# Performance work log

Hardware: AMD Instinct MI355X
Metric: run time of the kernel (lower is better)

The kernel has to match this reference:

```python
import jax, jax.numpy as jnp
import numpy as np

B, N, C, H = 64, 197, 768, 12
CH = C // H            # 64 head dim
RC = CH // 2           # 32 reduced channel
RN = N // 8            # 24 reduced tokens
TOPK_COEF = 8
BUDGET = int(np.ceil(0.25 * N))   # 50
BASIS_THRESH = 0.02
MP_SCALE = H ** -0.5               # MaskPredictor: num_heads**-0.5 (as in source)
ATTN_SCALE = CH ** -0.5
LN_EPS = 1e-5


def _ln(x, g, b):
    mu = x.mean(-1, keepdims=True)
    var = ((x - mu) ** 2).mean(-1, keepdims=True)
    return (x - mu) * jax.lax.rsqrt(var + LN_EPS) * g + b


def _keep_topk(x, k):
    # zero all but the k largest along last axis (tie-break by value threshold)
    kth = jax.lax.top_k(x, k)[0][..., -1:]
    return jnp.where(x >= kth, x, 0.0)


def setup_inputs() -> dict:
    key = jax.random.key(0)
    ks = jax.random.split(key, 20)
    d = {}
    d['x'] = jax.random.normal(ks[0], (B, N, C), jnp.float32)
    s = 0.02
    d['Wqkv'] = jax.random.normal(ks[1], (C, 3 * C), jnp.float32) * s
    d['Wcq'] = jax.random.normal(ks[2], (CH, RC), jnp.float32) * s
    d['bcq'] = jnp.zeros((RC,), jnp.float32)
    d['Wck'] = jax.random.normal(ks[3], (CH, RC), jnp.float32) * s
    d['bck'] = jnp.zeros((RC,), jnp.float32)
    d['proj_n'] = jax.random.normal(ks[4], (N, RN), jnp.float32) * s
    d['proj_back_n'] = jax.random.normal(ks[5], (N, RN), jnp.float32) * s
    d['Wproj'] = jax.random.normal(ks[6], (C, C), jnp.float32) * s
    d['bproj'] = jnp.zeros((C,), jnp.float32)
    d['g1'] = jnp.ones((C,), jnp.float32)
    d['b1'] = jnp.zeros((C,), jnp.float32)
    d['g2'] = jnp.ones((C,), jnp.float32)
    d['b2'] = jnp.zeros((C,), jnp.float32)
    d['W1'] = jax.random.normal(ks[7], (C, 4 * C), jnp.float32) * s
    d['bfc1'] = jnp.zeros((4 * C,), jnp.float32)
    d['W2'] = jax.random.normal(ks[8], (4 * C, C), jnp.float32) * s
    d['bfc2'] = jnp.zeros((C,), jnp.float32)
    return d


def reference(x, Wqkv, Wcq, bcq, Wck, bck, proj_n, proj_back_n, Wproj, bproj,
              g1, b1, g2, b2, W1, bfc1, W2, bfc2):
    h = _ln(x, g1, b1)
    qkv = (h @ Wqkv).reshape(B, N, 3, H, CH).transpose(2, 0, 3, 1, 4)  # [3,B,H,N,CH]
    q, k, v = qkv[0], qkv[1], qkv[2]

    # ---- MaskPredictor (eval path) ----
    qp = q @ Wcq + bcq                                # [B,H,N,RC]
    kp = k @ Wck + bck                                # [B,H,N,RC]
    kk = jnp.einsum('bhnc,nr->bhcr', kp, proj_n)      # [B,H,RC,RN]
    cheap = jnp.einsum('bhnc,bhcr->bhnr', qp, kk) * MP_SCALE
    cheap = cheap[:, :, 1:, :]                        # drop cls query row
    basis_coef = jax.nn.softmax(cheap, axis=-1)       # [B,H,N-1,RN]
    basis_coef = _keep_topk(basis_coef, TOPK_COEF)
    basis = jnp.abs(proj_back_n.T)                    # [RN,N]
    basis = jnp.where(basis > BASIS_THRESH, basis, 0.0)
    approx_attn = basis_coef @ basis                  # [B,H,N-1,N]
    kth = jax.lax.top_k(approx_attn, BUDGET)[0][..., -1:]
    mask = approx_attn >= kth                         # [B,H,N-1,N] bool
    cls_mask = jnp.ones((B, H, 1, N), bool)
    attn_mask = jnp.concatenate([cls_mask, mask], axis=2)  # [B,H,N,N]

    # ---- masked full attention ----
    attn = jnp.einsum('bhqc,bhkc->bhqk', q * ATTN_SCALE, k)
    attn = jnp.where(attn_mask, attn, -jnp.inf)
    attn = jax.nn.softmax(attn, axis=-1)
    out = jnp.einsum('bhqk,bhkc->bhqc', attn, v)
    out = out.transpose(0, 2, 1, 3).reshape(B, N, C)
    out = out @ Wproj + bproj

    x = x + out                                       # skip_lam = 1.0
    h2 = _ln(x, g2, b2)
    mlp = jax.nn.gelu(h2 @ W1 + bfc1, approximate=False) @ W2 + bfc2
    x = x + mlp
    return x
```

## Files before the change

kernel.cpp:

```cpp
#include <hip/hip_runtime.h>
#include <math.h>
#include <float.h>

#define B_ 64
#define N_ 197
#define C_ 768
#define H_ 12
#define CH_ 64
#define RC_ 32
#define RN_ 24

typedef __attribute__((ext_vector_type(8))) short short8;
typedef __attribute__((ext_vector_type(4))) float f32x4;
typedef __attribute__((address_space(3))) void  lds_void;
typedef __attribute__((address_space(1))) const void g_void;

__device__ __forceinline__ float warp_sum(float v){
  #pragma unroll
  for(int o=32;o>=1;o>>=1) v += __shfl_xor(v,o);
  return v;
}
__device__ __forceinline__ float warp_max(float v){
  #pragma unroll
  for(int o=32;o>=1;o>>=1) v = fmaxf(v,__shfl_xor(v,o));
  return v;
}
__device__ __forceinline__ unsigned short f2bf(float f){
  union{float f; unsigned u;} c; c.f = f;
  unsigned r = c.u + 0x7FFF + ((c.u>>16)&1);
  return (unsigned short)(r>>16);
}
__device__ __forceinline__ float bf2f(unsigned short u){
  union{unsigned u; float f;} c; c.u = ((unsigned)u)<<16; return c.f;
}

__global__ __launch_bounds__(256) void ln_kernel(const float* __restrict__ x,
    const float* __restrict__ g, const float* __restrict__ bb, unsigned short* __restrict__ out){
  int r = blockIdx.x; int tid = threadIdx.x;
  const float* xr = x + (size_t)r*C_;
  float v0=xr[tid], v1=xr[tid+256], v2=xr[tid+512];
  __shared__ float red[8];
  float s = warp_sum(v0+v1+v2);
  if((tid&63)==0) red[tid>>6]=s;
  __syncthreads();
  float mu = (red[0]+red[1]+red[2]+red[3]) * (1.f/768.f);
  float d0=v0-mu,d1=v1-mu,d2=v2-mu;
  float s2 = warp_sum(d0*d0+d1*d1+d2*d2);
  if((tid&63)==0) red[4+(tid>>6)]=s2;
  __syncthreads();
  float rinv = rsqrtf((red[4]+red[5]+red[6]+red[7])*(1.f/768.f)+1e-5f);
  unsigned short* orow = out + (size_t)r*C_;
  orow[tid]     = f2bf(d0*rinv*g[tid]    +bb[tid]);
  orow[tid+256] = f2bf(d1*rinv*g[tid+256]+bb[tid+256]);
  orow[tid+512] = f2bf(d2*rinv*g[tid+512]+bb[tid+512]);
}

__global__ __launch_bounds__(256) void wtrans_kernel(const float* __restrict__ in,
    unsigned short* __restrict__ out, int K, int N){
  __shared__ float tile[32][33];
  int n0 = blockIdx.x*32, k0 = blockIdx.y*32;
  int tx = threadIdx.x&31, ty = threadIdx.x>>5;
  #pragma unroll
  for(int i=0;i<4;++i) tile[ty+8*i][tx] = in[(size_t)(k0+ty+8*i)*N + n0+tx];
  __syncthreads();
  #pragma unroll
  for(int i=0;i<4;++i) out[(size_t)(n0+ty+8*i)*K + k0+tx] = f2bf(tile[tx][ty+8*i]);
}

template<int ACT, int RESID, int OUTBF16>
__global__ __launch_bounds__(256) void gemm_bf16(
    const unsigned short* __restrict__ A, const unsigned short* __restrict__ WT,
    const float* __restrict__ bias, const float* __restrict__ resid,
    void* __restrict__ Cout, int M, int K, int Nc){
  __shared__ unsigned short As[2*128*32];
  __shared__ unsigned short Bs[2*128*32];
  int tid = threadIdx.x, lane = tid&63, wid = tid>>6;
  int m0 = blockIdx.y*128, n0 = blockIdx.x*128;
  int wr = wid>>1, wc = wid&1;
  int lm = lane&15, lg = lane>>4;
  int row0 = tid>>2,         kc0 = (tid&3)*8;
  int row1 = (256+tid)>>2,   kc1 = (tid&3)*8;
  int ar0 = m0+row0; if(ar0 > M-1) ar0 = M-1;
  int ar1 = m0+row1; if(ar1 > M-1) ar1 = M-1;
  const unsigned short* gA0 = A  + (size_t)ar0*K + kc0;
  const unsigned short* gA1 = A  + (size_t)ar1*K + kc1;
  const unsigned short* gB0 = WT + (size_t)(n0+row0)*K + kc0;
  const unsigned short* gB1 = WT + (size_t)(n0+row1)*K + kc1;
  unsigned short* lA0 = As + (wid*64)*8;
  unsigned short* lA1 = As + (256 + wid*64)*8;
  unsigned short* lB0 = Bs + (wid*64)*8;
  unsigned short* lB1 = Bs + (256 + wid*64)*8;

#define STAGE_(buf, kt) do{ \
    __builtin_amdgcn_global_load_lds((g_void*)(gA0 + (kt)), (lds_void*)(lA0 + (buf)*4096), 16, 0, 0); \
    __builtin_amdgcn_global_load_lds((g_void*)(gB0 + (kt)), (lds_void*)(lB0 + (buf)*4096), 16, 0, 0); \
    __builtin_amdgcn_global_load_lds((g_void*)(gA1 + (kt)), (lds_void*)(lA1 + (buf)*4096), 16, 0, 0); \
    __builtin_amdgcn_global_load_lds((g_void*)(gB1 + (kt)), (lds_void*)(lB1 + (buf)*4096), 16, 0, 0); \
  }while(0)

  f32x4 acc[4][4] = {};
  const int nt = K/32;
  STAGE_(0, 0);
  __syncthreads();
  for(int t=0; t<nt; t+=2){
    STAGE_(1, (t+1)*32);
    {
      short8 af[4], bfv[4];
      #pragma unroll
      for(int i=0;i<4;++i){
        af[i]  = *(const short8*)(As + (64*wr + 16*i + lm)*32 + lg*8);
        bfv[i] = *(const short8*)(Bs + (64*wc + 16*i + lm)*32 + lg*8);
      }
      #pragma unroll
      for(int i=0;i<4;++i)
        #pragma unroll
        for(int j=0;j<4;++j)
          acc[i][j] = __builtin_amdgcn_mfma_f32_16x16x32_bf16(af[i], bfv[j], acc[i][j], 0,0,0);
    }
    __syncthreads();
    if(t+2 < nt) STAGE_(0, (t+2)*32);
    {
      short8 af[4], bfv[4];
      #pragma unroll
      for(int i=0;i<4;++i){
        af[i]  = *(const short8*)(As + 4096 + (64*wr + 16*i + lm)*32 + lg*8);
        bfv[i] = *(const short8*)(Bs + 4096 + (64*wc + 16*i + lm)*32 + lg*8);
      }
      #pragma unroll
      for(int i=0;i<4;++i)
        #pragma unroll
        for(int j=0;j<4;++j)
          acc[i][j] = __builtin_amdgcn_mfma_f32_16x16x32_bf16(af[i], bfv[j], acc[i][j], 0,0,0);
    }
    __syncthreads();
  }
#undef STAGE_
  #pragma unroll
  for(int i=0;i<4;++i){
    #pragma unroll
    for(int j=0;j<4;++j){
      int gcol = n0 + 64*wc + 16*j + lm;
      float bv = bias ? bias[gcol] : 0.f;
      #pragma unroll
      for(int r=0;r<4;++r){
        int grow = m0 + 64*wr + 16*i + lg*4 + r;
        if(grow < M){
          float cv = acc[i][j][r] + bv;
          if(ACT==1){
            float xx = cv;
            float p = xx*fmaf(xx*xx, 0.10294517f, 2.3022079f);
            float q = exp2f(p);
            cv = xx - xx*__builtin_amdgcn_rcpf(1.0f+q);
          }
          if(RESID) cv += resid[(size_t)grow*Nc + gcol];
          if(OUTBF16) ((unsigned short*)Cout)[(size_t)grow*Nc+gcol] = f2bf(cv);
          else        ((float*)Cout)[(size_t)grow*Nc+gcol] = cv;
        }
      }
    }
  }
}

__global__ __launch_bounds__(512) void cheap_kernel(
    const unsigned short* __restrict__ qkv,
    const float* __restrict__ Wcq, const float* __restrict__ bcq,
    const float* __restrict__ Wck, const float* __restrict__ bck,
    const float* __restrict__ proj_n, float* __restrict__ coef){
  int bh = blockIdx.x; int b = bh/H_, h = bh%H_;
  int tid = threadIdx.x, lane = tid&63, wv = tid>>6;
  __shared__ unsigned short KQ[197*64];
  __shared__ float P2[197*32];
  __shared__ float PN[197*24];
  __shared__ float KK[32*24];
  const unsigned short* Kbase = qkv + ((size_t)(b*N_)*3 + 1)*C_ + h*CH_;
  const unsigned short* Qbase = qkv + ((size_t)(b*N_)*3 + 0)*C_ + h*CH_;
  for(int idx = tid; idx < 197*32; idx += 512){
    int k = idx>>5, cp = (idx&31)*2;
    *(unsigned*)&KQ[k*64+cp] = *(const unsigned*)(Kbase + (size_t)k*3*C_ + cp);
  }
  for(int idx = tid; idx < 4728; idx += 512) PN[idx]=proj_n[idx];
  __syncthreads();
  int mycol = tid&31;
  {
    float wreg[64];
    #pragma unroll 64
    for(int c=0;c<64;++c) wreg[c] = Wck[c*32+mycol];
    float bias = bck[mycol];
    for(int idx = tid; idx < 197*32; idx += 512){
      int n = idx>>5;
      float acc = bias;
      const uint4* krow = (const uint4*)(KQ + n*64);
      #pragma unroll
      for(int q8=0;q8<8;++q8){
        uint4 u4 = krow[q8];
        unsigned uu[4] = {u4.x,u4.y,u4.z,u4.w};
        #pragma unroll
        for(int p2=0;p2<4;++p2){
          float lo = __uint_as_float(uu[p2]<<16);
          float hi = __uint_as_float(uu[p2]&0xffff0000u);
          acc += lo*wreg[q8*8+p2*2];
          acc += hi*wreg[q8*8+p2*2+1];
        }
      }
      P2[idx] = acc;
    }
  }
  __syncthreads();
  {
    int i0 = tid, i1 = tid+512;
    int c0 = i0/24, r0 = i0-c0*24;
    int c1 = (i1<768)? i1/24 : 0;
    int r1 = (i1<768)? i1-c1*24 : 0;
    float a0=0.f, a1=0.f;
    for(int n=0;n<197;++n){
      float pn0 = PN[n*24+r0];
      a0 += P2[n*32+c0]*pn0;
      if(i1<768) a1 += P2[n*32+c1]*PN[n*24+r1];
    }
    if(i0<768) KK[i0]=a0;
    if(i1<768) KK[i1]=a1;
    for(int idx = tid; idx < 197*32; idx += 512){
      int k = idx>>5, cp = (idx&31)*2;
      *(unsigned*)&KQ[k*64+cp] = *(const unsigned*)(Qbase + (size_t)k*3*C_ + cp);
    }
  }
  __syncthreads();
  {
    float wreg[64];
    #pragma unroll 64
    for(int c=0;c<64;++c) wreg[c] = Wcq[c*32+mycol];
    float bias = bcq[mycol];
    for(int idx = tid; idx < 197*32; idx += 512){
      int n = idx>>5;
      float acc = bias;
      const uint4* krow = (const uint4*)(KQ + n*64);
      #pragma unroll
      for(int q8=0;q8<8;++q8){
        uint4 u4 = krow[q8];
        unsigned uu[4] = {u4.x,u4.y,u4.z,u4.w};
        #pragma unroll
        for(int p2=0;p2<4;++p2){
          float lo = __uint_as_float(uu[p2]<<16);
          float hi = __uint_as_float(uu[p2]&0xffff0000u);
          acc += lo*wreg[q8*8+p2*2];
          acc += hi*wreg[q8*8+p2*2+1];
        }
      }
      P2[idx] = acc;
    }
  }
  __syncthreads();
  bool act = lane < RN_;
  int ll = act ? lane : 0;
  float kkreg[32];
  #pragma unroll
  for(int c=0;c<32;++c) kkreg[c] = KK[c*24 + ll];
  for(int i = wv; i < 196; i += 8){
    int n = i+1;
    float pr[32];
    #pragma unroll
    for(int q=0;q<8;++q){
      float4 v4 = *(const float4*)&P2[n*32 + q*4];
      pr[q*4]=v4.x; pr[q*4+1]=v4.y; pr[q*4+2]=v4.z; pr[q*4+3]=v4.w;
    }
    float accv = 0.f;
    #pragma unroll
    for(int c=0;c<32;++c) accv += pr[c]*kkreg[c];
    float val = act ? accv * 0.28867513459481287f : -INFINITY;
    float m = warp_max(val);
    float e = act ? expf(val-m) : 0.f;
    float ssum = warp_sum(e);
    float p = e/ssum;
    unsigned u = __float_as_uint(e);
    unsigned prefix = 0;
    #pragma unroll
    for(int bit=30; bit>=0; --bit){
      unsigned t = prefix | (1u<<bit);
      int c = __popcll(__ballot(u >= t));
      if(c >= 8) prefix = t;
    }
    if(act) coef[((size_t)bh*196 + i)*24 + lane] = (u >= prefix) ? p : 0.f;
  }
}

__global__ __launch_bounds__(256) void basis_kernel(const float* __restrict__ pb,
    float* __restrict__ basis){
  int t = blockIdx.x*256 + threadIdx.x;
  if(t < RN_*N_){
    int r = t/N_, j = t%N_;
    float v = fabsf(pb[(size_t)j*RN_ + r]);
    basis[t] = (v > 0.02f) ? v : 0.f;
  }
}

__global__ __launch_bounds__(256) void mask4_kernel(const float* __restrict__ coef,
    const float* __restrict__ basis, unsigned int* __restrict__ maskw){
  __shared__ float Bs[24*256];
  int tid = threadIdx.x, lane = tid&63, wv = tid>>6;
  for(int idx = tid; idx < 24*256; idx += 256){
    int r = idx>>8, q = idx&255;
    int e = ((q&3)<<6) | (q>>2);
    Bs[idx] = (e < N_) ? basis[r*N_ + e] : 0.f;
  }
  __syncthreads();
  int rowbase = blockIdx.x*16 + wv*4;
  #pragma unroll
  for(int j=0;j<4;++j){
    int row = rowbase + j;
    int qi = row % N_; int bh = row / N_;
    if(qi==0){
      if(lane<8){
        unsigned v = (lane<6)?0xFFFFFFFFu:((lane==6)?0x1Fu:0u);
        maskw[(size_t)row*8+lane]=v;
      }
      continue;
    }
    float cfv = (lane<24) ? coef[((size_t)bh*196 + (qi-1))*24 + lane] : 0.f;
    unsigned long long nz = __ballot(cfv != 0.f);
    float4 av = make_float4(0.f,0.f,0.f,0.f);
    while(nz){
      int r = __ffsll((unsigned long long)nz) - 1;
      nz &= nz - 1;
      float c = __uint_as_float(__builtin_amdgcn_readlane(__float_as_uint(cfv), r));
      float4 bv = *(const float4*)&Bs[r*256 + lane*4];
      av.x += c*bv.x; av.y += c*bv.y; av.z += c*bv.z; av.w += c*bv.w;
    }
    unsigned u0=__float_as_uint(av.x), u1=__float_as_uint(av.y);
    unsigned u2=__float_as_uint(av.z), u3=__float_as_uint(av.w);
    unsigned prefix = 0;
    #pragma unroll
    for(int bit=30; bit>=0; --bit){
      unsigned t = prefix | (1u<<bit);
      int c = __popcll(__ballot(u0 >= t)) + __popcll(__ballot(u1 >= t))
            + __popcll(__ballot(u2 >= t)) + __popcll(__ballot(u3 >= t));
      if(c >= 50) prefix = t;
    }
    unsigned uu[4] = {u0,u1,u2,u3};
    #pragma unroll
    for(int r=0;r<4;++r){
      bool valid = (r<3) | (lane<5);
      bool keep = valid && (uu[r] >= prefix);
      unsigned long long bal = __ballot(keep);
      if(lane==0){
        maskw[(size_t)row*8 + 2*r]   = (unsigned)(bal & 0xFFFFFFFFull);
        maskw[(size_t)row*8 + 2*r+1] = (unsigned)(bal>>32);
      }
    }
  }
}

__global__ __launch_bounds__(512) void attn3_kernel(const unsigned short* __restrict__ qkv,
    const unsigned int* __restrict__ maskw, unsigned short* __restrict__ attn_out){
  int bh = blockIdx.x; int b = bh/H_, h = bh%H_;
  int tid = threadIdx.x, lane = tid&63, wv = tid>>6;
  int g = lane>>4, c16 = lane&15;
  __shared__ unsigned short Kb[208*64];
  __shared__ unsigned short Vt[64*220];
  __shared__ unsigned short Pl[8*16*224];
  __shared__ unsigned int   Ml[8][16][8];
  const unsigned short* Kbase = qkv + ((size_t)(b*N_)*3 + 1)*C_ + h*CH_;
  const unsigned short* Vbase = qkv + ((size_t)(b*N_)*3 + 2)*C_ + h*CH_;
  for(int idx = tid; idx < 208*32; idx += 512){
    int k = idx>>5, cp = idx&31;
    unsigned pk = 0;
    if(k < N_) pk = *(const unsigned*)(Kbase + (size_t)k*3*C_ + cp*2);
    unsigned off = (unsigned)(k*128 + cp*4) ^ ((unsigned)(k&7)<<4);
    *(unsigned*)((char*)Kb + off) = pk;
  }
  for(int idx = tid; idx < 64*110; idx += 512){
    int kp = idx>>6, c = idx&63;
    int k0 = kp*2, k1 = kp*2+1;
    unsigned v0 = (k0<N_) ? Vbase[(size_t)k0*3*C_ + c] : 0;
    unsigned v1 = (k1<N_) ? Vbase[(size_t)k1*3*C_ + c] : 0;
    *(unsigned*)((char*)Vt + c*440 + kp*4) = v0 | (v1<<16);
  }
  __syncthreads();
  size_t pbase = (size_t)wv*16*448;
  for(int i=lane;i<128;i+=64){
    int ql = i>>3; int kk = 208 + (i&7)*2;
    unsigned off = (unsigned)(ql*448 + kk*2) ^ ((unsigned)(ql&7)<<4);
    *(unsigned*)((char*)Pl + pbase + off) = 0u;
  }
  for(int t = wv; t < 13; t += 8){
    int qb = t*16;
    for(int i = lane; i < 128; i += 64){
      int row = i>>3, word = i&7;
      int qr = qb+row; if(qr>196) qr=196;
      Ml[wv][row][word] = maskw[(size_t)(bh*N_+qr)*8 + word];
    }
    int qrow = qb + c16; if(qrow>196) qrow=196;
    const unsigned short* Qr = qkv + ((size_t)(b*N_+qrow)*3)*C_ + h*CH_ + g*8;
    short8 af[2];
    af[0] = *(const short8*)(Qr);
    af[1] = *(const short8*)(Qr + 32);
    f32x4 sf[13];
    #pragma unroll
    for(int f=0;f<13;++f){
      sf[f] = (f32x4){0.f,0.f,0.f,0.f};
      #pragma unroll
      for(int s=0;s<2;++s){
        int row = f*16 + c16;
        unsigned off = (unsigned)(row*128 + s*64 + g*16) ^ ((unsigned)(row&7)<<4);
        short8 bfr = *(const short8*)((char*)Kb + off);
        sf[f] = __builtin_amdgcn_mfma_f32_16x16x32_bf16(af[s], bfr, sf[f], 0,0,0);
      }
      sf[f][0]*=0.125f; sf[f][1]*=0.125f; sf[f][2]*=0.125f; sf[f][3]*=0.125f;
    }
    unsigned keep[4] = {0,0,0,0};
    float m[4] = {-FLT_MAX,-FLT_MAX,-FLT_MAX,-FLT_MAX};
    #pragma unroll
    for(int f=0;f<13;++f)
      #pragma unroll
      for(int r=0;r<4;++r){
        unsigned bit = (Ml[wv][g*4+r][f>>1] >> ((f&1)*16 + c16)) & 1u;
        keep[r] |= bit<<f;
        if(bit) m[r] = fmaxf(m[r], sf[f][r]);
      }
    #pragma unroll
    for(int r=0;r<4;++r){
      #pragma unroll
      for(int o=8;o>=1;o>>=1) m[r] = fmaxf(m[r], __shfl_xor(m[r], o));
    }
    float sum[4] = {0,0,0,0};
    #pragma unroll
    for(int f=0;f<13;++f)
      #pragma unroll
      for(int r=0;r<4;++r){
        float e = ((keep[r]>>f)&1u) ? expf(sf[f][r]-m[r]) : 0.f;
        sf[f][r] = e; sum[r] += e;
      }
    #pragma unroll
    for(int r=0;r<4;++r){
      #pragma unroll
      for(int o=8;o>=1;o>>=1) sum[r] += __shfl_xor(sum[r], o);
      sum[r] = 1.f/sum[r];
    }
    #pragma unroll
    for(int f=0;f<13;++f)
      #pragma unroll
      for(int r=0;r<4;++r){
        int ql = g*4+r;
        unsigned off = (unsigned)(ql*448 + (f*16+c16)*2) ^ ((unsigned)(ql&7)<<4);
        *(unsigned short*)((char*)Pl + pbase + off) = f2bf(sf[f][r]*sum[r]);
      }
    #pragma unroll
    for(int ct=0;ct<4;++ct){
      f32x4 oa = (f32x4){0.f,0.f,0.f,0.f};
      #pragma unroll
      for(int ks=0;ks<7;++ks){
        unsigned offa = (unsigned)(c16*448 + (ks*32+g*8)*2) ^ ((unsigned)(c16&7)<<4);
        short8 pa = *(const short8*)((char*)Pl + pbase + offa);
        short8 vb = *(const short8*)((char*)Vt + (size_t)(ct*16+c16)*440 + (ks*32+g*8)*2);
        oa = __builtin_amdgcn_mfma_f32_16x16x32_bf16(pa, vb, oa, 0,0,0);
      }
      #pragma unroll
      for(int r=0;r<4;++r){
        int qq = qb + g*4 + r;
        if(qq < N_)
          attn_out[((size_t)(b*N_+qq))*C_ + h*CH_ + ct*16 + c16] = f2bf(oa[r]);
      }
    }
  }
}

extern "C" void kernel_launch(void* const* d_in, const int* in_sizes, int n_in,
                              void* d_out, int out_size, void* d_ws, size_t ws_size,
                              hipStream_t stream){
  const float* x    =(const float*)d_in[0];
  const float* Wqkv =(const float*)d_in[1];
  const float* Wcq  =(const float*)d_in[2];
  const float* bcq  =(const float*)d_in[3];
  const float* Wck  =(const float*)d_in[4];
  const float* bck  =(const float*)d_in[5];
  const float* proj_n=(const float*)d_in[6];
  const float* proj_back_n=(const float*)d_in[7];
  const float* Wproj=(const float*)d_in[8];
  const float* bproj=(const float*)d_in[9];
  const float* g1=(const float*)d_in[10];
  const float* b1=(const float*)d_in[11];
  const float* g2=(const float*)d_in[12];
  const float* b2=(const float*)d_in[13];
  const float* W1=(const float*)d_in[14];
  const float* bfc1=(const float*)d_in[15];
  const float* W2=(const float*)d_in[16];
  const float* bfc2=(const float*)d_in[17];
  float* out=(float*)d_out;

  float* ws=(float*)d_ws;
  size_t off=0;
  unsigned short* hbuf = (unsigned short*)(ws+off); off += (size_t)12608*768/2;
  size_t qkv_off = off;
  unsigned short* qkv = (unsigned short*)(ws+off); off += (size_t)12608*2304/2;
  off += (size_t)768*197*32;
  off += (size_t)768*197*32;
  off += (size_t)768*32*24;
  float* coef = ws+off;        off += (size_t)768*196*24;
  float* basis= ws+off;        off += 4736;
  unsigned int* maskw=(unsigned int*)(ws+off); off += (size_t)768*197*8;
  unsigned short* WqkvT = (unsigned short*)(ws+off); off += (size_t)2304*768/2;
  unsigned short* WprojT= (unsigned short*)(ws+off); off += (size_t)768*768/2;
  unsigned short* W1T   = (unsigned short*)(ws+off); off += (size_t)3072*768/2;
  unsigned short* W2T   = (unsigned short*)(ws+off); off += (size_t)768*3072/2;
  unsigned short* attn_out = hbuf;
  unsigned short* hidden = (unsigned short*)(ws+qkv_off);
  float* x1 = out;

  wtrans_kernel<<<dim3(72,24),256,0,stream>>>(Wqkv, WqkvT, 768, 2304);
  wtrans_kernel<<<dim3(24,24),256,0,stream>>>(Wproj, WprojT, 768, 768);
  wtrans_kernel<<<dim3(96,24),256,0,stream>>>(W1, W1T, 768, 3072);
  wtrans_kernel<<<dim3(24,96),256,0,stream>>>(W2, W2T, 3072, 768);
  ln_kernel<<<12608,256,0,stream>>>(x,g1,b1,hbuf);
  gemm_bf16<0,0,1><<<dim3(18,99),256,0,stream>>>(hbuf,WqkvT,nullptr,nullptr,qkv,12608,768,2304);
  cheap_kernel<<<768,512,0,stream>>>(qkv,Wcq,bcq,Wck,bck,proj_n,coef);
  basis_kernel<<<19,256,0,stream>>>(proj_back_n,basis);
  mask4_kernel<<<9456,256,0,stream>>>(coef,basis,maskw);
  attn3_kernel<<<768,512,0,stream>>>(qkv,maskw,attn_out);
  gemm_bf16<0,1,0><<<dim3(6,99),256,0,stream>>>(attn_out,WprojT,bproj,x,x1,12608,768,768);
  ln_kernel<<<12608,256,0,stream>>>(x1,g2,b2,hbuf);
  gemm_bf16<1,0,1><<<dim3(24,99),256,0,stream>>>(hbuf,W1T,bfc1,nullptr,hidden,12608,768,3072);
  gemm_bf16<0,1,0><<<dim3(6,99),256,0,stream>>>(hidden,W2T,bfc2,x1,out,12608,3072,768);
}
```

Before: 762.2 us.

## Use MFMA for cheap-kernel channel projections and pack two rows per wave

The per-(batch,head) mask predictor kernel now computes the q/k reduced-channel projections with bf16 MFMA instructions, reading from a swizzled LDS tile of K/Q. The weights are pre-transposed to bf16 by a small prep kernel. The projected keys are stored transposed so the token-reduction dot product uses float4 LDS loads. The coefficient softmax/top-k stage now handles two query rows per wave with 32-lane reductions. This targets the scalar FMA cost and idle lanes in the cheap_kernel. In exchange it adds a launch, and rounding the small weights to bf16 could shift which mask entries fall at the top-k boundary.

```diff
diff --git a/kernel.cpp b/kernel.cpp
--- a/kernel.cpp
+++ b/kernel.cpp
@@ -65,6 +65,17 @@
   __syncthreads();
   #pragma unroll
   for(int i=0;i<4;++i) out[(size_t)(n0+ty+8*i)*K + k0+tx] = f2bf(tile[tx][ty+8*i]);
+}
+
+__global__ __launch_bounds__(256) void wcprep_kernel(const float* __restrict__ Wcq,
+    const float* __restrict__ Wck, unsigned short* __restrict__ WcqT,
+    unsigned short* __restrict__ WckT){
+  int t = blockIdx.x*256 + threadIdx.x;
+  if(t < 2048){
+    int c = t>>6, k = t&63;
+    WcqT[t] = f2bf(Wcq[k*32+c]);
+    WckT[t] = f2bf(Wck[k*32+c]);
+  }
 }
 
 template<int ACT, int RESID, int OUTBF16>
@@ -163,123 +174,147 @@
 
 __global__ __launch_bounds__(512) void cheap_kernel(
     const unsigned short* __restrict__ qkv,
-    const float* __restrict__ Wcq, const float* __restrict__ bcq,
-    const float* __restrict__ Wck, const float* __restrict__ bck,
+    const unsigned short* __restrict__ WcqT, const float* __restrict__ bcq,
+    const unsigned short* __restrict__ WckT, const float* __restrict__ bck,
     const float* __restrict__ proj_n, float* __restrict__ coef){
   int bh = blockIdx.x; int b = bh/H_, h = bh%H_;
   int tid = threadIdx.x, lane = tid&63, wv = tid>>6;
-  __shared__ unsigned short KQ[197*64];
-  __shared__ float P2[197*32];
-  __shared__ float PN[197*24];
-  __shared__ float KK[32*24];
+  int lm = lane&15, lg = lane>>4;
+  __shared__ __align__(16) unsigned short KQ[208*64];
+  __shared__ __align__(16) float P2T[32*212];
+  __shared__ __align__(16) float PNT[24*200];
+  __shared__ float KK[768];
   const unsigned short* Kbase = qkv + ((size_t)(b*N_)*3 + 1)*C_ + h*CH_;
   const unsigned short* Qbase = qkv + ((size_t)(b*N_)*3 + 0)*C_ + h*CH_;
-  for(int idx = tid; idx < 197*32; idx += 512){
-    int k = idx>>5, cp = (idx&31)*2;
-    *(unsigned*)&KQ[k*64+cp] = *(const unsigned*)(Kbase + (size_t)k*3*C_ + cp);
-  }
-  for(int idx = tid; idx < 4728; idx += 512) PN[idx]=proj_n[idx];
-  __syncthreads();
-  int mycol = tid&31;
+  for(int idx = tid; idx < 208*32; idx += 512){
+    int k = idx>>5, cp = idx&31;
+    unsigned v = (k < N_) ? *(const unsigned*)(Kbase + (size_t)k*3*C_ + cp*2) : 0u;
+    unsigned off = (unsigned)(k*128 + cp*4) ^ ((unsigned)(k&7)<<4);
+    *(unsigned*)((char*)KQ + off) = v;
+  }
+  for(int idx = tid; idx < 24*200; idx += 512){
+    int r = idx/200, n = idx - r*200;
+    PNT[idx] = (n < N_) ? proj_n[n*24+r] : 0.f;
+  }
+  __syncthreads();
   {
-    float wreg[64];
-    #pragma unroll 64
-    for(int c=0;c<64;++c) wreg[c] = Wck[c*32+mycol];
-    float bias = bck[mycol];
+    short8 bfr[2][2];
+    #pragma unroll
+    for(int j=0;j<2;++j)
+      #pragma unroll
+      for(int s=0;s<2;++s)
+        bfr[j][s] = *(const short8*)(WckT + (j*16+lm)*64 + s*32 + lg*8);
+    float bias[2] = { bck[lm], bck[16+lm] };
+    for(int t=wv; t<13; t+=8){
+      int row = t*16 + lm;
+      unsigned o0 = (unsigned)(row*128 + lg*16) ^ ((unsigned)(row&7)<<4);
+      unsigned o1 = (unsigned)(row*128 + 64 + lg*16) ^ ((unsigned)(row&7)<<4);
+      short8 a0 = *(const short8*)((char*)KQ + o0);
+      short8 a1 = *(const short8*)((char*)KQ + o1);
+      #pragma unroll
+      for(int j=0;j<2;++j){
+        f32x4 acc = (f32x4){0.f,0.f,0.f,0.f};
+        acc = __builtin_amdgcn_mfma_f32_16x16x32_bf16(a0, bfr[j][0], acc, 0,0,0);
+        acc = __builtin_amdgcn_mfma_f32_16x16x32_bf16(a1, bfr[j][1], acc, 0,0,0);
+        #pragma unroll
+        for(int r=0;r<4;++r)
+          P2T[(j*16+lm)*212 + t*16 + lg*4 + r] = acc[r] + bias[j];
+      }
+    }
+  }
+  __syncthreads();
+  {
+    int i0 = tid, i1 = tid + 512;
+    bool has1 = (i1 < 768);
+    int c0 = i0/24, r0 = i0 - c0*24;
+    int c1 = has1 ? i1/24 : 0, r1 = has1 ? (i1 - (i1/24)*24) : 0;
+    float a0=0.f, a1=0.f;
+    for(int n=0;n<200;n+=4){
+      float4 x0 = *(const float4*)&P2T[c0*212+n];
+      float4 p0 = *(const float4*)&PNT[r0*200+n];
+      a0 += x0.x*p0.x; a0 += x0.y*p0.y; a0 += x0.z*p0.z; a0 += x0.w*p0.w;
+      if(has1){
+        float4 x1 = *(const float4*)&P2T[c1*212+n];
+        float4 p1 = *(const float4*)&PNT[r1*200+n];
+        a1 += x1.x*p1.x; a1 += x1.y*p1.y; a1 += x1.z*p1.z; a1 += x1.w*p1.w;
+      }
+    }
+    KK[i0] = a0;
+    if(has1) KK[i1] = a1;
     for(int idx = tid; idx < 197*32; idx += 512){
-      int n = idx>>5;
-      float acc = bias;
-      const uint4* krow = (const uint4*)(KQ + n*64);
-      #pragma unroll
-      for(int q8=0;q8<8;++q8){
-        uint4 u4 = krow[q8];
-        unsigned uu[4] = {u4.x,u4.y,u4.z,u4.w};
+      int k = idx>>5, cp = idx&31;
+      unsigned v = *(const unsigned*)(Qbase + (size_t)k*3*C_ + cp*2);
+      unsigned off = (unsigned)(k*128 + cp*4) ^ ((unsigned)(k&7)<<4);
+      *(unsigned*)((char*)KQ + off) = v;
+    }
+  }
+  __syncthreads();
+  float* QP = P2T;
+  {
+    short8 bfr[2][2];
+    #pragma unroll
+    for(int j=0;j<2;++j)
+      #pragma unroll
+      for(int s=0;s<2;++s)
+        bfr[j][s] = *(const short8*)(WcqT + (j*16+lm)*64 + s*32 + lg*8);
+    float bias[2] = { bcq[lm], bcq[16+lm] };
+    for(int t=wv; t<13; t+=8){
+      int row = t*16 + lm;
+      unsigned o0 = (unsigned)(row*128 + lg*16) ^ ((unsigned)(row&7)<<4);
+      unsigned o1 = (unsigned)(row*128 + 64 + lg*16) ^ ((unsigned)(row&7)<<4);
+      short8 a0 = *(const short8*)((char*)KQ + o0);
+      short8 a1 = *(const short8*)((char*)KQ + o1);
+      #pragma unroll
+      for(int j=0;j<2;++j){
+        f32x4 acc = (f32x4){0.f,0.f,0.f,0.f};
+        acc = __builtin_amdgcn_mfma_f32_16x16x32_bf16(a0, bfr[j][0], acc, 0,0,0);
+        acc = __builtin_amdgcn_mfma_f32_16x16x32_bf16(a1, bfr[j][1], acc, 0,0,0);
         #pragma unroll
-        for(int p2=0;p2<4;++p2){
-          float lo = __uint_as_float(uu[p2]<<16);
-          float hi = __uint_as_float(uu[p2]&0xffff0000u);
-          acc += lo*wreg[q8*8+p2*2];
-          acc += hi*wreg[q8*8+p2*2+1];
-        }
-      }
-      P2[idx] = acc;
-    }
-  }
-  __syncthreads();
-  {
-    int i0 = tid, i1 = tid+512;
-    int c0 = i0/24, r0 = i0-c0*24;
-    int c1 = (i1<768)? i1/24 : 0;
-    int r1 = (i1<768)? i1-c1*24 : 0;
-    float a0=0.f, a1=0.f;
-    for(int n=0;n<197;++n){
-      float pn0 = PN[n*24+r0];
-      a0 += P2[n*32+c0]*pn0;
-      if(i1<768) a1 += P2[n*32+c1]*PN[n*24+r1];
-    }
-    if(i0<768) KK[i0]=a0;
-    if(i1<768) KK[i1]=a1;
-    for(int idx = tid; idx < 197*32; idx += 512){
-      int k = idx>>5, cp = (idx&31)*2;
-      *(unsigned*)&KQ[k*64+cp] = *(const unsigned*)(Qbase + (size_t)k*3*C_ + cp);
-    }
-  }
-  __syncthreads();
-  {
-    float wreg[64];
-    #pragma unroll 64
-    for(int c=0;c<64;++c) wreg[c] = Wcq[c*32+mycol];
-    float bias = bcq[mycol];
-    for(int idx = tid; idx < 197*32; idx += 512){
-      int n = idx>>5;
-      float acc = bias;
-      const uint4* krow = (const uint4*)(KQ + n*64);
-      #pragma unroll
-      for(int q8=0;q8<8;++q8){
-        uint4 u4 = krow[q8];
-        unsigned uu[4] = {u4.x,u4.y,u4.z,u4.w};
-        #pragma unroll
-        for(int p2=0;p2<4;++p2){
-          float lo = __uint_as_float(uu[p2]<<16);
-          float hi = __uint_as_float(uu[p2]&0xffff0000u);
-          acc += lo*wreg[q8*8+p2*2];
-          acc += hi*wreg[q8*8+p2*2+1];
-        }
-      }
-      P2[idx] = acc;
-    }
-  }
-  __syncthreads();
-  bool act = lane < RN_;
-  int ll = act ? lane : 0;
+        for(int r=0;r<4;++r)
+          QP[(t*16 + lg*4 + r)*32 + j*16 + lm] = acc[r] + bias[j];
+      }
+    }
+  }
+  __syncthreads();
+  int l32 = lane & 31, half = lane >> 5;
+  bool act = l32 < RN_;
+  int ll = act ? l32 : 0;
   float kkreg[32];
   #pragma unroll
   for(int c=0;c<32;++c) kkreg[c] = KK[c*24 + ll];
-  for(int i = wv; i < 196; i += 8){
-    int n = i+1;
-    float pr[32];
+  for(int i2 = wv*2; i2 < 196; i2 += 16){
+    int i = i2 + half;
+    int n = i + 1;
+    float accv = 0.f;
     #pragma unroll
     for(int q=0;q<8;++q){
-      float4 v4 = *(const float4*)&P2[n*32 + q*4];
-      pr[q*4]=v4.x; pr[q*4+1]=v4.y; pr[q*4+2]=v4.z; pr[q*4+3]=v4.w;
-    }
-    float accv = 0.f;
-    #pragma unroll
-    for(int c=0;c<32;++c) accv += pr[c]*kkreg[c];
+      float4 v4 = *(const float4*)&QP[n*32 + q*4];
+      accv += v4.x*kkreg[q*4];   accv += v4.y*kkreg[q*4+1];
+      accv += v4.z*kkreg[q*4+2]; accv += v4.w*kkreg[q*4+3];
+    }
     float val = act ? accv * 0.28867513459481287f : -INFINITY;
-    float m = warp_max(val);
-    float e = act ? expf(val-m) : 0.f;
-    float ssum = warp_sum(e);
+    float m = val;
+    #pragma unroll
+    for(int o=16;o>=1;o>>=1) m = fmaxf(m, __shfl_xor(m, o));
+    float e = act ? expf(val - m) : 0.f;
+    float ssum = e;
+    #pragma unroll
+    for(int o=16;o>=1;o>>=1) ssum += __shfl_xor(ssum, o);
     float p = e/ssum;
     unsigned u = __float_as_uint(e);
-    unsigned prefix = 0;
+    unsigned pL=0, pH=0;
     #pragma unroll
     for(int bit=30; bit>=0; --bit){
-      unsigned t = prefix | (1u<<bit);
-      int c = __popcll(__ballot(u >= t));
-      if(c >= 8) prefix = t;
-    }
-    if(act) coef[((size_t)bh*196 + i)*24 + lane] = (u >= prefix) ? p : 0.f;
+      unsigned tL = pL | (1u<<bit), tH = pH | (1u<<bit);
+      unsigned thr = half ? tH : tL;
+      unsigned long long bal = __ballot(u >= thr);
+      int cL = __popcll(bal & 0xFFFFFFull);
+      int cH = __popcll((bal>>32) & 0xFFFFFFull);
+      if(cL>=8) pL=tL;
+      if(cH>=8) pH=tH;
+    }
+    unsigned myp = half ? pH : pL;
+    if(act) coef[((size_t)bh*196 + i)*24 + l32] = (u >= myp) ? p : 0.f;
   }
 }
 
@@ -501,6 +536,8 @@
   unsigned short* WprojT= (unsigned short*)(ws+off); off += (size_t)768*768/2;
   unsigned short* W1T   = (unsigned short*)(ws+off); off += (size_t)3072*768/2;
   unsigned short* W2T   = (unsigned short*)(ws+off); off += (size_t)768*3072/2;
+  unsigned short* WcqT  = (unsigned short*)(ws+off); off += 1024;
+  unsigned short* WckT  = (unsigned short*)(ws+off); off += 1024;
   unsigned short* attn_out = hbuf;
   unsigned short* hidden = (unsigned short*)(ws+qkv_off);
   float* x1 = out;
@@ -509,9 +546,10 @@
   wtrans_kernel<<<dim3(24,24),256,0,stream>>>(Wproj, WprojT, 768, 768);
   wtrans_kernel<<<dim3(96,24),256,0,stream>>>(W1, W1T, 768, 3072);
   wtrans_kernel<<<dim3(24,96),256,0,stream>>>(W2, W2T, 3072, 768);
+  wcprep_kernel<<<8,256,0,stream>>>(Wcq, Wck, WcqT, WckT);
   ln_kernel<<<12608,256,0,stream>>>(x,g1,b1,hbuf);
   gemm_bf16<0,0,1><<<dim3(18,99),256,0,stream>>>(hbuf,WqkvT,nullptr,nullptr,qkv,12608,768,2304);
-  cheap_kernel<<<768,512,0,stream>>>(qkv,Wcq,bcq,Wck,bck,proj_n,coef);
+  cheap_kernel<<<768,512,0,stream>>>(qkv,WcqT,bcq,WckT,bck,proj_n,coef);
   basis_kernel<<<19,256,0,stream>>>(proj_back_n,basis);
   mask4_kernel<<<9456,256,0,stream>>>(coef,basis,maskw);
   attn3_kernel<<<768,512,0,stream>>>(qkv,maskw,attn_out);
```

After: 725.4 us. -4.8%, faster.
